# Performance work log

Hardware: AMD Instinct MI355X
Metric: run time of the kernel (lower is better)

## Reference

```python
import jax, jax.numpy as jnp
import numpy as np

N_NODES = 50000
N_EDGES = 800000
HID = 256
OUT = 128
NEG_SLOPE = 0.2


def gat_layer(x, src, dst, W_src, W_dst, a_src_vec, a_dst_vec, bias, n_nodes):
    # Dense projections (PyG lin_src / lin_dst for tuple in_channels)
    h_src = x @ W_src              # [N, C]
    h_dst = x @ W_dst              # [N, C]
    # Per-node attention logits (att_src/att_dst dot products)
    a_src = h_src @ a_src_vec      # [N]
    a_dst = h_dst @ a_dst_vec      # [N]
    # Edge logits + LeakyReLU
    e = jax.nn.leaky_relu(a_src[src] + a_dst[dst], NEG_SLOPE)  # [E]
    # Segment softmax over incoming edges of each dst node
    m = jax.ops.segment_max(e, dst, num_segments=n_nodes)      # [N]
    m = jnp.where(jnp.isfinite(m), m, 0.0)                      # empty segments
    ex = jnp.exp(e - m[dst])                                    # [E]
    s = jax.ops.segment_sum(ex, dst, num_segments=n_nodes)     # [N]
    alpha = ex / (s[dst] + 1e-16)                               # [E]
    # Attention-weighted message aggregation (scatter-add to dst)
    msg = alpha[:, None] * h_src[src]                           # [E, C]
    out = jax.ops.segment_sum(msg, dst, num_segments=n_nodes)  # [N, C]
    return out + bias


def setup_inputs() -> dict:
    key = jax.random.key(0)
    ks = jax.random.split(key, 12)
    x = jax.random.normal(ks[0], (N_NODES, HID), dtype=jnp.float32)
    edge_index = jax.random.randint(ks[1], (2, N_EDGES), 0, N_NODES, dtype=jnp.int64)
    sc1 = 1.0 / np.sqrt(HID)
    sc2 = 1.0 / np.sqrt(HID)
    return {
        "x": x,
        "edge_index": edge_index,
        "W1_src": jax.random.normal(ks[2], (HID, HID), dtype=jnp.float32) * sc1,
        "W1_dst": jax.random.normal(ks[3], (HID, HID), dtype=jnp.float32) * sc1,
        "att1_src": jax.random.normal(ks[4], (HID,), dtype=jnp.float32) * sc1,
        "att1_dst": jax.random.normal(ks[5], (HID,), dtype=jnp.float32) * sc1,
        "b1": jnp.zeros((HID,), dtype=jnp.float32),
        "W2_src": jax.random.normal(ks[6], (HID, OUT), dtype=jnp.float32) * sc2,
        "W2_dst": jax.random.normal(ks[7], (HID, OUT), dtype=jnp.float32) * sc2,
        "att2_src": jax.random.normal(ks[8], (OUT,), dtype=jnp.float32) * (1.0 / np.sqrt(OUT)),
        "att2_dst": jax.random.normal(ks[9], (OUT,), dtype=jnp.float32) * (1.0 / np.sqrt(OUT)),
        "b2": jnp.zeros((OUT,), dtype=jnp.float32),
    }


def reference(x, edge_index, W1_src, W1_dst, att1_src, att1_dst, b1,
              W2_src, W2_dst, att2_src, att2_dst, b2):
    src, dst = edge_index[0], edge_index[1]
    h = gat_layer(x, src, dst, W1_src, W1_dst, att1_src, att1_dst, b1, N_NODES)
    h = jax.nn.relu(h)
    out = gat_layer(h, src, dst, W2_src, W2_dst, att2_src, att2_dst, b2, N_NODES)
    return out
```

## Files before the change

kernel.cpp:

```cpp
#include <hip/hip_runtime.h>
#include <math.h>

#define N_NODES 50000
#define N_EDGES 800000
#define HID 256
#define OUT_C 128
#define NEG_SLOPE 0.2f
#define SCAN_NB ((N_NODES + 255) / 256)

typedef __attribute__((ext_vector_type(8))) short bf16x8;
typedef __attribute__((ext_vector_type(4))) float f32x4;
typedef _Float16 half_t;
typedef __attribute__((ext_vector_type(4))) _Float16 half4;
typedef __attribute__((ext_vector_type(2))) _Float16 half2t;

__device__ inline unsigned short bf16_rne(float x) {
    unsigned u = __float_as_uint(x);
    return (unsigned short)((u + 0x7fffu + ((u >> 16) & 1u)) >> 16);
}


__global__ __launch_bounds__(256) void hist_rank_kernel(
    const int* __restrict__ dst, int* __restrict__ counts, int* __restrict__ rank) {
    int e = blockIdx.x * 256 + threadIdx.x;
    if (e < N_EDGES) rank[e] = atomicAdd(&counts[dst[e]], 1);
}

__global__ __launch_bounds__(256) void block_scan_kernel(
    const int* __restrict__ counts, int* __restrict__ excl,
    int* __restrict__ blockSums, int n) {
    __shared__ int waveSums[4];
    int i = blockIdx.x * 256 + threadIdx.x;
    int lane = threadIdx.x & 63;
    int wv = threadIdx.x >> 6;
    int c = (i < n) ? counts[i] : 0;
    int v = c;
    #pragma unroll
    for (int off = 1; off < 64; off <<= 1) {
        int t = __shfl_up(v, off);
        if (lane >= off) v += t;
    }
    if (lane == 63) waveSums[wv] = v;
    __syncthreads();
    int waveOff = 0;
    #pragma unroll
    for (int w = 0; w < 4; w++)
        if (w < wv) waveOff += waveSums[w];
    if (i < n) excl[i] = waveOff + v - c;
    if (threadIdx.x == 255) blockSums[blockIdx.x] = waveOff + v;
}

__global__ __launch_bounds__(256) void add_offsets_kernel(
    int* __restrict__ excl, const int* __restrict__ blockSums, int n) {
    __shared__ int lds[4];
    int tid = threadIdx.x;
    int partial = 0;
    for (int j = tid; j < (int)blockIdx.x; j += 256) partial += blockSums[j];
    #pragma unroll
    for (int off = 32; off > 0; off >>= 1) partial += __shfl_down(partial, off);
    if ((tid & 63) == 0) lds[tid >> 6] = partial;
    __syncthreads();
    int prefix = lds[0] + lds[1] + lds[2] + lds[3];
    int i = blockIdx.x * 256 + tid;
    if (i < n) excl[i] += prefix;
    if (i == 0) excl[n] = N_EDGES;
}

__global__ __launch_bounds__(256) void scatter_kernel(
    const int* __restrict__ src, const int* __restrict__ dst,
    const int* __restrict__ offsets, const int* __restrict__ rank,
    int* __restrict__ src_sorted) {
    int e = blockIdx.x * 256 + threadIdx.x;
    if (e >= N_EDGES) return;
    src_sorted[offsets[dst[e]] + rank[e]] = src[e];
}


__global__ __launch_bounds__(64) void compute_v_all_kernel(
    const float* __restrict__ W1s, const float* __restrict__ att1s,
    const float* __restrict__ W1d, const float* __restrict__ att1d,
    const float* __restrict__ W2s, const float* __restrict__ att2s,
    const float* __restrict__ W2d, const float* __restrict__ att2d,
    float* __restrict__ v1s, float* __restrict__ v1d,
    float* __restrict__ v2s, float* __restrict__ v2d) {
    int k = blockIdx.x;
    int lane = threadIdx.x;
    const float* W; const float* att; float* v; int cout;
    switch (blockIdx.y) {
        case 0: W = W1s; att = att1s; v = v1s; cout = HID; break;
        case 1: W = W1d; att = att1d; v = v1d; cout = HID; break;
        case 2: W = W2s; att = att2s; v = v2s; cout = OUT_C; break;
        default: W = W2d; att = att2d; v = v2d; cout = OUT_C; break;
    }
    float sum = 0.f;
    for (int j = lane; j < cout; j += 64)
        sum += W[k * cout + j] * att[j];
    #pragma unroll
    for (int off = 32; off > 0; off >>= 1)
        sum += __shfl_down(sum, off);
    if (lane == 0) v[k] = sum;
}


#define PACK1_T (8 * 17 * 64)
#define PACK2_T (8 * 9 * 64)

__global__ __launch_bounds__(256) void pack_all_kernel(
    const float* __restrict__ W1, const float* __restrict__ v1s, const float* __restrict__ v1d,
    const float* __restrict__ W2, const float* __restrict__ v2s, const float* __restrict__ v2d,
    unsigned short* __restrict__ hi1, unsigned short* __restrict__ lo1,
    unsigned short* __restrict__ hi2, unsigned short* __restrict__ lo2) {
    int t = blockIdx.x * 256 + threadIdx.x;
    const float *W, *vs, *vd; unsigned short *hi, *lo; int cout, NTL, tt;
    if (t < PACK1_T)            { tt = t;           W = W1; vs = v1s; vd = v1d; hi = hi1; lo = lo1; cout = HID;  NTL = 17; }
    else if (t < PACK1_T + PACK2_T) { tt = t - PACK1_T; W = W2; vs = v2s; vd = v2d; hi = hi2; lo = lo2; cout = OUT_C; NTL = 9; }
    else return;
    int lane = tt & 63;
    int tile = (tt >> 6) % NTL;
    int ks = tt / (64 * NTL);
    int m = lane & 15;
    int kbase = ks * 32 + (lane >> 4) * 8;
    #pragma unroll
    for (int j = 0; j < 8; j++) {
        float val;
        if (tile < NTL - 1) val = W[(kbase + j) * cout + tile * 16 + m];
        else val = (m == 0) ? vs[kbase + j] : (m == 1) ? vd[kbase + j] : 0.f;
        unsigned short h = bf16_rne(val);
        hi[tt * 8 + j] = h;
        lo[tt * 8 + j] = bf16_rne(val - __uint_as_float((unsigned)h << 16));
    }
}


template <int COUT, int NT, bool WRITE_A>
__device__ __forceinline__ void gemm_body(
    const float* __restrict__ A, const unsigned short* __restrict__ Bhi,
    const unsigned short* __restrict__ Blo, half_t* __restrict__ H,
    float* __restrict__ a_s, float* __restrict__ a_d, int M, int tile0) {
    const int NTL = COUT / 16 + 1;
    int wave = threadIdx.x >> 6, lane = threadIdx.x & 63;
    int m = lane & 15, quad = lane >> 4;
    int row0 = blockIdx.x * 128 + wave * 32;
    f32x4 acc[2][NT];
    #pragma unroll
    for (int rg = 0; rg < 2; rg++)
        #pragma unroll
        for (int nt = 0; nt < NT; nt++)
            acc[rg][nt] = (f32x4){0.f, 0.f, 0.f, 0.f};

    const float* arow[2];
    #pragma unroll
    for (int rg = 0; rg < 2; rg++) {
        int r = row0 + rg * 16 + m;
        if (r >= M) r = M - 1;
        arow[rg] = A + (size_t)r * HID;
    }

    for (int ks = 0; ks < 8; ks++) {
        bf16x8 ah[2], al[2];
        #pragma unroll
        for (int rg = 0; rg < 2; rg++) {
            const float* ap = arow[rg] + ks * 32 + quad * 8;
            float4 v0 = *(const float4*)ap;
            float4 v1 = *(const float4*)(ap + 4);
            float av[8] = {v0.x, v0.y, v0.z, v0.w, v1.x, v1.y, v1.z, v1.w};
            #pragma unroll
            for (int j = 0; j < 8; j++) {
                unsigned short h = bf16_rne(av[j]);
                float hf = __uint_as_float((unsigned)h << 16);
                ah[rg][j] = (short)h;
                al[rg][j] = (short)bf16_rne(av[j] - hf);
            }
        }
        #pragma unroll
        for (int nt = 0; nt < NT; nt++) {
            int tile = (WRITE_A && nt == NT - 1) ? (COUT / 16) : (tile0 + nt);
            size_t fbase = ((size_t)(ks * NTL + tile) * 64 + lane) * 8;
            bf16x8 bh = *(const bf16x8*)(Bhi + fbase);
            bf16x8 bl = *(const bf16x8*)(Blo + fbase);
            acc[0][nt] = __builtin_amdgcn_mfma_f32_16x16x32_bf16(ah[0], bh, acc[0][nt], 0, 0, 0);
            acc[1][nt] = __builtin_amdgcn_mfma_f32_16x16x32_bf16(ah[1], bh, acc[1][nt], 0, 0, 0);
            acc[0][nt] = __builtin_amdgcn_mfma_f32_16x16x32_bf16(ah[0], bl, acc[0][nt], 0, 0, 0);
            acc[1][nt] = __builtin_amdgcn_mfma_f32_16x16x32_bf16(ah[1], bl, acc[1][nt], 0, 0, 0);
            acc[0][nt] = __builtin_amdgcn_mfma_f32_16x16x32_bf16(al[0], bh, acc[0][nt], 0, 0, 0);
            acc[1][nt] = __builtin_amdgcn_mfma_f32_16x16x32_bf16(al[1], bh, acc[1][nt], 0, 0, 0);
        }
    }
    const int NW = WRITE_A ? NT - 1 : NT;
    #pragma unroll
    for (int rg = 0; rg < 2; rg++)
        #pragma unroll
        for (int nt = 0; nt < NW; nt++)
            #pragma unroll
            for (int r = 0; r < 4; r++) {
                int row = row0 + rg * 16 + quad * 4 + r;
                if (row < M)
                    H[(size_t)row * COUT + (tile0 + nt) * 16 + m] = (half_t)acc[rg][nt][r];
            }
    if (WRITE_A) {
        #pragma unroll
        for (int rg = 0; rg < 2; rg++)
            #pragma unroll
            for (int r = 0; r < 4; r++) {
                int row = row0 + rg * 16 + quad * 4 + r;
                if (row < M) {
                    if (m == 0) a_s[row] = acc[rg][NT - 1][r];
                    else if (m == 1) a_d[row] = acc[rg][NT - 1][r];
                }
            }
    }
}

template <int COUT>
__global__ __launch_bounds__(256) void mfma_gemm_a_kernel(
    const float* __restrict__ A, const unsigned short* __restrict__ Bhi,
    const unsigned short* __restrict__ Blo, half_t* __restrict__ H,
    float* __restrict__ a_s, float* __restrict__ a_d, int M) {
    if (blockIdx.y == 0)
        gemm_body<COUT, 9, true>(A, Bhi, Blo, H, a_s, a_d, M, 0);
    else
        gemm_body<COUT, 8, false>(A, Bhi, Blo, H, a_s, a_d, M, 8);
}


template <int C, bool RELU>
__global__ __launch_bounds__(256) void fused_aggregate_kernel(
    const int* __restrict__ offsets, const int* __restrict__ src_sorted,
    const float* __restrict__ a_src, const float* __restrict__ a_dst,
    const half_t* __restrict__ h, const float* __restrict__ bias,
    float* __restrict__ out) {
    constexpr int CH = 8;
    int node = (int)((blockIdx.x * 256u + threadIdx.x) >> 6);
    int lane = threadIdx.x & 63;
    if (node >= N_NODES) return;
    int beg = offsets[node], end = offsets[node + 1];
    float ad = a_dst[node];
    float s = 0.f;

    if (C == 256) {
        float4 acc = make_float4(0.f, 0.f, 0.f, 0.f);
        for (int base = beg; base < end; base += CH) {
            int cnt = end - base; if (cnt > CH) cnt = CH;
            int idx[CH];
            #pragma unroll
            for (int j = 0; j < CH; j++)
                idx[j] = src_sorted[(j < cnt) ? base + j : base];
            half4 hv[CH];
            #pragma unroll
            for (int j = 0; j < CH; j++)
                hv[j] = *(const half4*)(h + (size_t)idx[j] * C + lane * 4);
            float w[CH];
            #pragma unroll
            for (int j = 0; j < CH; j++) {
                float l = a_src[idx[j]] + ad;
                if (l < 0.f) l *= NEG_SLOPE;
                w[j] = (j < cnt) ? expf(l) : 0.f;
                s += w[j];
            }
            #pragma unroll
            for (int j = 0; j < CH; j++) {
                acc.x += w[j] * (float)hv[j][0]; acc.y += w[j] * (float)hv[j][1];
                acc.z += w[j] * (float)hv[j][2]; acc.w += w[j] * (float)hv[j][3];
            }
        }
        float inv = 1.f / (s + 1e-16f);
        float4 bv = *(const float4*)(bias + lane * 4);
        acc.x = acc.x * inv + bv.x; acc.y = acc.y * inv + bv.y;
        acc.z = acc.z * inv + bv.z; acc.w = acc.w * inv + bv.w;
        if (RELU) {
            acc.x = fmaxf(acc.x, 0.f); acc.y = fmaxf(acc.y, 0.f);
            acc.z = fmaxf(acc.z, 0.f); acc.w = fmaxf(acc.w, 0.f);
        }
        *(float4*)(out + (size_t)node * C + lane * 4) = acc;
    } else {
        float2 acc = make_float2(0.f, 0.f);
        for (int base = beg; base < end; base += CH) {
            int cnt = end - base; if (cnt > CH) cnt = CH;
            int idx[CH];
            #pragma unroll
            for (int j = 0; j < CH; j++)
                idx[j] = src_sorted[(j < cnt) ? base + j : base];
            half2t hv[CH];
            #pragma unroll
            for (int j = 0; j < CH; j++)
                hv[j] = *(const half2t*)(h + (size_t)idx[j] * C + lane * 2);
            float w[CH];
            #pragma unroll
            for (int j = 0; j < CH; j++) {
                float l = a_src[idx[j]] + ad;
                if (l < 0.f) l *= NEG_SLOPE;
                w[j] = (j < cnt) ? expf(l) : 0.f;
                s += w[j];
            }
            #pragma unroll
            for (int j = 0; j < CH; j++) {
                acc.x += w[j] * (float)hv[j][0]; acc.y += w[j] * (float)hv[j][1];
            }
        }
        float inv = 1.f / (s + 1e-16f);
        float2 bv = *(const float2*)(bias + lane * 2);
        acc.x = acc.x * inv + bv.x; acc.y = acc.y * inv + bv.y;
        if (RELU) { acc.x = fmaxf(acc.x, 0.f); acc.y = fmaxf(acc.y, 0.f); }
        *(float2*)(out + (size_t)node * C + lane * 2) = acc;
    }
}

extern "C" void kernel_launch(void* const* d_in, const int* in_sizes, int n_in,
                              void* d_out, int out_size, void* d_ws, size_t ws_size,
                              hipStream_t stream) {
    const float* x     = (const float*)d_in[0];
    const int*   edge  = (const int*)d_in[1];
    const int*   src   = edge;
    const int*   dst   = edge + N_EDGES;
    const float* W1s   = (const float*)d_in[2];
    const float* W1d   = (const float*)d_in[3];
    const float* att1s = (const float*)d_in[4];
    const float* att1d = (const float*)d_in[5];
    const float* b1    = (const float*)d_in[6];
    const float* W2s   = (const float*)d_in[7];
    const float* W2d   = (const float*)d_in[8];
    const float* att2s = (const float*)d_in[9];
    const float* att2d = (const float*)d_in[10];
    const float* b2    = (const float*)d_in[11];
    float* out = (float*)d_out;

    float* ws    = (float*)d_ws;
    half_t* h1   = (half_t*)ws;
    float* act2  = ws + (size_t)N_NODES * HID;
    float* a_s   = act2 + (size_t)N_NODES * HID;
    float* a_d   = a_s + N_NODES;
    float* vbuf  = a_d + N_NODES;
    int* ibase      = (int*)(vbuf + 4 * HID);
    int* src_sorted = ibase;
    int* rank       = src_sorted + N_EDGES;
    int* counts     = rank + N_EDGES;
    int* offsets    = counts + N_NODES;
    int* blockSums  = offsets + N_NODES + 1;
    unsigned short* wp1h = (unsigned short*)(((uintptr_t)(blockSums + SCAN_NB) + 15) & ~(uintptr_t)15);
    unsigned short* wp1l = wp1h + PACK1_T * 8;
    unsigned short* wp2h = wp1l + PACK1_T * 8;
    unsigned short* wp2l = wp2h + PACK2_T * 8;
    float* v1s = vbuf, *v1d = vbuf + HID, *v2s = vbuf + 2 * HID, *v2d = vbuf + 3 * HID;
    half_t* h2 = h1;

    const int edgeBlocks = (N_EDGES + 255) / 256;
    const int waveBlocksN = (N_NODES + 3) / 4;
    const int gemmBlocks = (N_NODES + 127) / 128;

    hipMemsetAsync(counts, 0, N_NODES * sizeof(int), stream);
    hist_rank_kernel<<<edgeBlocks, 256, 0, stream>>>(dst, counts, rank);
    block_scan_kernel<<<SCAN_NB, 256, 0, stream>>>(counts, offsets, blockSums, N_NODES);
    add_offsets_kernel<<<SCAN_NB, 256, 0, stream>>>(offsets, blockSums, N_NODES);
    scatter_kernel<<<edgeBlocks, 256, 0, stream>>>(src, dst, offsets, rank, src_sorted);

    compute_v_all_kernel<<<dim3(HID, 4), 64, 0, stream>>>(
        W1s, att1s, W1d, att1d, W2s, att2s, W2d, att2d, v1s, v1d, v2s, v2d);
    pack_all_kernel<<<(PACK1_T + PACK2_T + 255) / 256, 256, 0, stream>>>(
        W1s, v1s, v1d, W2s, v2s, v2d, wp1h, wp1l, wp2h, wp2l);

    mfma_gemm_a_kernel<HID><<<dim3(gemmBlocks, 2), 256, 0, stream>>>(
        x, wp1h, wp1l, h1, a_s, a_d, N_NODES);
    fused_aggregate_kernel<HID, true><<<waveBlocksN, 256, 0, stream>>>(
        offsets, src_sorted, a_s, a_d, h1, b1, act2);

    mfma_gemm_a_kernel<OUT_C><<<dim3(gemmBlocks, 1), 256, 0, stream>>>(
        act2, wp2h, wp2l, h2, a_s, a_d, N_NODES);
    fused_aggregate_kernel<OUT_C, false><<<waveBlocksN, 256, 0, stream>>>(
        offsets, src_sorted, a_s, a_d, h2, b2, out);
}
```

Measured before the change: 339.6 us.

## Stage GEMM weights in LDS, store hidden activations as fp16, use fast exp

The GEMM kernel now runs as one block per 128 rows covering all output tiles. Each k-step copies the packed bf16 hi/lo weight fragments into shared memory, so waves read them from LDS instead of global memory. The layer-1 aggregate writes its activations as fp16, which halves the traffic for writing them and for the second GEMM reading them. The aggregation loops drop the per-chunk clamp by padding src_sorted with zeros and switch expf to __expf. The costs are extra barriers, more accumulator registers per wave (17 tiles) that may lower occupancy, and fp16 rounding of the intermediate activations.

```diff
diff --git a/kernel.cpp b/kernel.cpp
--- a/kernel.cpp
+++ b/kernel.cpp
@@ -11,6 +11,7 @@
 typedef __attribute__((ext_vector_type(8))) short bf16x8;
 typedef __attribute__((ext_vector_type(4))) float f32x4;
 typedef _Float16 half_t;
+typedef __attribute__((ext_vector_type(8))) _Float16 half8;
 typedef __attribute__((ext_vector_type(4))) _Float16 half4;
 typedef __attribute__((ext_vector_type(2))) _Float16 half2t;
 
@@ -73,6 +74,7 @@
     int e = blockIdx.x * 256 + threadIdx.x;
     if (e >= N_EDGES) return;
     src_sorted[offsets[dst[e]] + rank[e]] = src[e];
+    if (e < 8) src_sorted[N_EDGES + e] = 0;
 }
 
 
@@ -132,23 +134,25 @@
 }
 
 
-template <int COUT, int NT, bool WRITE_A>
-__device__ __forceinline__ void gemm_body(
-    const float* __restrict__ A, const unsigned short* __restrict__ Bhi,
+template <int COUT, typename AT>
+__global__ __launch_bounds__(256) void mfma_gemm_a_kernel(
+    const AT* __restrict__ A, const unsigned short* __restrict__ Bhi,
     const unsigned short* __restrict__ Blo, half_t* __restrict__ H,
-    float* __restrict__ a_s, float* __restrict__ a_d, int M, int tile0) {
-    const int NTL = COUT / 16 + 1;
-    int wave = threadIdx.x >> 6, lane = threadIdx.x & 63;
+    float* __restrict__ a_s, float* __restrict__ a_d, int M) {
+    constexpr int NTL = COUT / 16 + 1;
+    __shared__ unsigned short ldsB[2 * NTL * 512];
+    int tid = threadIdx.x;
+    int wave = tid >> 6, lane = tid & 63;
     int m = lane & 15, quad = lane >> 4;
     int row0 = blockIdx.x * 128 + wave * 32;
-    f32x4 acc[2][NT];
+    f32x4 acc[2][NTL];
     #pragma unroll
     for (int rg = 0; rg < 2; rg++)
         #pragma unroll
-        for (int nt = 0; nt < NT; nt++)
+        for (int nt = 0; nt < NTL; nt++)
             acc[rg][nt] = (f32x4){0.f, 0.f, 0.f, 0.f};
 
-    const float* arow[2];
+    const AT* arow[2];
     #pragma unroll
     for (int rg = 0; rg < 2; rg++) {
         int r = row0 + rg * 16 + m;
@@ -157,13 +161,28 @@
     }
 
     for (int ks = 0; ks < 8; ks++) {
+        const uint4* sh = (const uint4*)(Bhi + (size_t)ks * NTL * 512);
+        const uint4* sl = (const uint4*)(Blo + (size_t)ks * NTL * 512);
+        uint4* d = (uint4*)ldsB;
+        for (int i = tid; i < NTL * 64; i += 256) {
+            d[i] = sh[i];
+            d[NTL * 64 + i] = sl[i];
+        }
         bf16x8 ah[2], al[2];
         #pragma unroll
         for (int rg = 0; rg < 2; rg++) {
-            const float* ap = arow[rg] + ks * 32 + quad * 8;
-            float4 v0 = *(const float4*)ap;
-            float4 v1 = *(const float4*)(ap + 4);
-            float av[8] = {v0.x, v0.y, v0.z, v0.w, v1.x, v1.y, v1.z, v1.w};
+            const AT* ap = arow[rg] + ks * 32 + quad * 8;
+            float av[8];
+            if constexpr (sizeof(AT) == 2) {
+                half8 hv = *(const half8*)ap;
+                #pragma unroll
+                for (int j = 0; j < 8; j++) av[j] = (float)hv[j];
+            } else {
+                float4 v0 = *(const float4*)ap;
+                float4 v1 = *(const float4*)(ap + 4);
+                av[0] = v0.x; av[1] = v0.y; av[2] = v0.z; av[3] = v0.w;
+                av[4] = v1.x; av[5] = v1.y; av[6] = v1.z; av[7] = v1.w;
+            }
             #pragma unroll
             for (int j = 0; j < 8; j++) {
                 unsigned short h = bf16_rne(av[j]);
@@ -172,12 +191,11 @@
                 al[rg][j] = (short)bf16_rne(av[j] - hf);
             }
         }
-        #pragma unroll
-        for (int nt = 0; nt < NT; nt++) {
-            int tile = (WRITE_A && nt == NT - 1) ? (COUT / 16) : (tile0 + nt);
-            size_t fbase = ((size_t)(ks * NTL + tile) * 64 + lane) * 8;
-            bf16x8 bh = *(const bf16x8*)(Bhi + fbase);
-            bf16x8 bl = *(const bf16x8*)(Blo + fbase);
+        __syncthreads();
+        #pragma unroll
+        for (int nt = 0; nt < NTL; nt++) {
+            bf16x8 bh = *(const bf16x8*)(ldsB + (nt * 64 + lane) * 8);
+            bf16x8 bl = *(const bf16x8*)(ldsB + NTL * 512 + (nt * 64 + lane) * 8);
             acc[0][nt] = __builtin_amdgcn_mfma_f32_16x16x32_bf16(ah[0], bh, acc[0][nt], 0, 0, 0);
             acc[1][nt] = __builtin_amdgcn_mfma_f32_16x16x32_bf16(ah[1], bh, acc[1][nt], 0, 0, 0);
             acc[0][nt] = __builtin_amdgcn_mfma_f32_16x16x32_bf16(ah[0], bl, acc[0][nt], 0, 0, 0);
@@ -185,50 +203,37 @@
             acc[0][nt] = __builtin_amdgcn_mfma_f32_16x16x32_bf16(al[0], bh, acc[0][nt], 0, 0, 0);
             acc[1][nt] = __builtin_amdgcn_mfma_f32_16x16x32_bf16(al[1], bh, acc[1][nt], 0, 0, 0);
         }
-    }
-    const int NW = WRITE_A ? NT - 1 : NT;
+        __syncthreads();
+    }
     #pragma unroll
     for (int rg = 0; rg < 2; rg++)
         #pragma unroll
-        for (int nt = 0; nt < NW; nt++)
+        for (int nt = 0; nt < NTL - 1; nt++)
             #pragma unroll
             for (int r = 0; r < 4; r++) {
                 int row = row0 + rg * 16 + quad * 4 + r;
                 if (row < M)
-                    H[(size_t)row * COUT + (tile0 + nt) * 16 + m] = (half_t)acc[rg][nt][r];
-            }
-    if (WRITE_A) {
-        #pragma unroll
-        for (int rg = 0; rg < 2; rg++)
-            #pragma unroll
-            for (int r = 0; r < 4; r++) {
-                int row = row0 + rg * 16 + quad * 4 + r;
-                if (row < M) {
-                    if (m == 0) a_s[row] = acc[rg][NT - 1][r];
-                    else if (m == 1) a_d[row] = acc[rg][NT - 1][r];
-                }
-            }
-    }
-}
-
-template <int COUT>
-__global__ __launch_bounds__(256) void mfma_gemm_a_kernel(
-    const float* __restrict__ A, const unsigned short* __restrict__ Bhi,
-    const unsigned short* __restrict__ Blo, half_t* __restrict__ H,
-    float* __restrict__ a_s, float* __restrict__ a_d, int M) {
-    if (blockIdx.y == 0)
-        gemm_body<COUT, 9, true>(A, Bhi, Blo, H, a_s, a_d, M, 0);
-    else
-        gemm_body<COUT, 8, false>(A, Bhi, Blo, H, a_s, a_d, M, 8);
-}
-
-
-template <int C, bool RELU>
+                    H[(size_t)row * COUT + nt * 16 + m] = (half_t)acc[rg][nt][r];
+            }
+    #pragma unroll
+    for (int rg = 0; rg < 2; rg++)
+        #pragma unroll
+        for (int r = 0; r < 4; r++) {
+            int row = row0 + rg * 16 + quad * 4 + r;
+            if (row < M) {
+                if (m == 0) a_s[row] = acc[rg][NTL - 1][r];
+                else if (m == 1) a_d[row] = acc[rg][NTL - 1][r];
+            }
+        }
+}
+
+
+template <int C, bool RELU, typename OT>
 __global__ __launch_bounds__(256) void fused_aggregate_kernel(
     const int* __restrict__ offsets, const int* __restrict__ src_sorted,
     const float* __restrict__ a_src, const float* __restrict__ a_dst,
     const half_t* __restrict__ h, const float* __restrict__ bias,
-    float* __restrict__ out) {
+    OT* __restrict__ out) {
     constexpr int CH = 8;
     int node = (int)((blockIdx.x * 256u + threadIdx.x) >> 6);
     int lane = threadIdx.x & 63;
@@ -240,11 +245,11 @@
     if (C == 256) {
         float4 acc = make_float4(0.f, 0.f, 0.f, 0.f);
         for (int base = beg; base < end; base += CH) {
-            int cnt = end - base; if (cnt > CH) cnt = CH;
+            int cnt = end - base;
             int idx[CH];
             #pragma unroll
             for (int j = 0; j < CH; j++)
-                idx[j] = src_sorted[(j < cnt) ? base + j : base];
+                idx[j] = src_sorted[base + j];
             half4 hv[CH];
             #pragma unroll
             for (int j = 0; j < CH; j++)
@@ -254,7 +259,7 @@
             for (int j = 0; j < CH; j++) {
                 float l = a_src[idx[j]] + ad;
                 if (l < 0.f) l *= NEG_SLOPE;
-                w[j] = (j < cnt) ? expf(l) : 0.f;
+                w[j] = (j < cnt) ? __expf(l) : 0.f;
                 s += w[j];
             }
             #pragma unroll
@@ -271,15 +276,20 @@
             acc.x = fmaxf(acc.x, 0.f); acc.y = fmaxf(acc.y, 0.f);
             acc.z = fmaxf(acc.z, 0.f); acc.w = fmaxf(acc.w, 0.f);
         }
-        *(float4*)(out + (size_t)node * C + lane * 4) = acc;
+        if constexpr (sizeof(OT) == 2) {
+            half4 o = { (half_t)acc.x, (half_t)acc.y, (half_t)acc.z, (half_t)acc.w };
+            *(half4*)(out + (size_t)node * C + lane * 4) = o;
+        } else {
+            *(float4*)(out + (size_t)node * C + lane * 4) = acc;
+        }
     } else {
         float2 acc = make_float2(0.f, 0.f);
         for (int base = beg; base < end; base += CH) {
-            int cnt = end - base; if (cnt > CH) cnt = CH;
+            int cnt = end - base;
             int idx[CH];
             #pragma unroll
             for (int j = 0; j < CH; j++)
-                idx[j] = src_sorted[(j < cnt) ? base + j : base];
+                idx[j] = src_sorted[base + j];
             half2t hv[CH];
             #pragma unroll
             for (int j = 0; j < CH; j++)
@@ -289,7 +299,7 @@
             for (int j = 0; j < CH; j++) {
                 float l = a_src[idx[j]] + ad;
                 if (l < 0.f) l *= NEG_SLOPE;
-                w[j] = (j < cnt) ? expf(l) : 0.f;
+                w[j] = (j < cnt) ? __expf(l) : 0.f;
                 s += w[j];
             }
             #pragma unroll
@@ -301,7 +311,12 @@
         float2 bv = *(const float2*)(bias + lane * 2);
         acc.x = acc.x * inv + bv.x; acc.y = acc.y * inv + bv.y;
         if (RELU) { acc.x = fmaxf(acc.x, 0.f); acc.y = fmaxf(acc.y, 0.f); }
-        *(float2*)(out + (size_t)node * C + lane * 2) = acc;
+        if constexpr (sizeof(OT) == 2) {
+            half2t o = { (half_t)acc.x, (half_t)acc.y };
+            *(half2t*)(out + (size_t)node * C + lane * 2) = o;
+        } else {
+            *(float2*)(out + (size_t)node * C + lane * 2) = acc;
+        }
     }
 }
 
@@ -324,19 +339,18 @@
     const float* b2    = (const float*)d_in[11];
     float* out = (float*)d_out;
 
-    float* ws    = (float*)d_ws;
-    half_t* h1   = (half_t*)ws;
-    float* act2  = ws + (size_t)N_NODES * HID;
-    float* a_s   = act2 + (size_t)N_NODES * HID;
-    float* a_d   = a_s + N_NODES;
-    float* vbuf  = a_d + N_NODES;
-    int* ibase      = (int*)(vbuf + 4 * HID);
-    int* src_sorted = ibase;
-    int* rank       = src_sorted + N_EDGES;
-    int* counts     = rank + N_EDGES;
-    int* offsets    = counts + N_NODES;
-    int* blockSums  = offsets + N_NODES + 1;
-    unsigned short* wp1h = (unsigned short*)(((uintptr_t)(blockSums + SCAN_NB) + 15) & ~(uintptr_t)15);
+    char* p = (char*)d_ws;
+    half_t* h1   = (half_t*)p; p += (size_t)N_NODES * HID * 2;
+    half_t* act2 = (half_t*)p; p += (size_t)N_NODES * HID * 2;
+    float* a_s   = (float*)p;  p += N_NODES * 4;
+    float* a_d   = (float*)p;  p += N_NODES * 4;
+    float* vbuf  = (float*)p;  p += 4 * HID * 4;
+    int* src_sorted = (int*)p; p += (N_EDGES + 8) * 4;
+    int* rank       = (int*)p; p += N_EDGES * 4;
+    int* counts     = (int*)p; p += N_NODES * 4;
+    int* offsets    = (int*)p; p += (N_NODES + 1) * 4;
+    int* blockSums  = (int*)p; p += SCAN_NB * 4;
+    unsigned short* wp1h = (unsigned short*)(((uintptr_t)p + 15) & ~(uintptr_t)15);
     unsigned short* wp1l = wp1h + PACK1_T * 8;
     unsigned short* wp2h = wp1l + PACK1_T * 8;
     unsigned short* wp2l = wp2h + PACK2_T * 8;
@@ -358,13 +372,13 @@
     pack_all_kernel<<<(PACK1_T + PACK2_T + 255) / 256, 256, 0, stream>>>(
         W1s, v1s, v1d, W2s, v2s, v2d, wp1h, wp1l, wp2h, wp2l);
 
-    mfma_gemm_a_kernel<HID><<<dim3(gemmBlocks, 2), 256, 0, stream>>>(
+    mfma_gemm_a_kernel<HID, float><<<gemmBlocks, 256, 0, stream>>>(
         x, wp1h, wp1l, h1, a_s, a_d, N_NODES);
-    fused_aggregate_kernel<HID, true><<<waveBlocksN, 256, 0, stream>>>(
+    fused_aggregate_kernel<HID, true, half_t><<<waveBlocksN, 256, 0, stream>>>(
         offsets, src_sorted, a_s, a_d, h1, b1, act2);
 
-    mfma_gemm_a_kernel<OUT_C><<<dim3(gemmBlocks, 1), 256, 0, stream>>>(
+    mfma_gemm_a_kernel<OUT_C, half_t><<<gemmBlocks, 256, 0, stream>>>(
         act2, wp2h, wp2l, h2, a_s, a_d, N_NODES);
-    fused_aggregate_kernel<OUT_C, false><<<waveBlocksN, 256, 0, stream>>>(
+    fused_aggregate_kernel<OUT_C, false, float><<<waveBlocksN, 256, 0, stream>>>(
         offsets, src_sorted, a_s, a_d, h2, b2, out);
 }
```

After: 348.5 us. 2.6% more time.
